# Kernel tuning notes

Measured on AMD Instinct MI355X. Metric: run time of the kernel, lower is better.

The kernel has to match this reference:

```python
import jax, jax.numpy as jnp
import numpy as np

N_NODES = 100000
EPS = 1e-12  # torch F.normalize eps


def setup_inputs() -> dict:
    key = jax.random.key(0)
    ks = jax.random.split(key, 8)
    F_IN, H, C, E = 128, 128, 8, 1600000
    s = 1.0 / np.sqrt(F_IN)
    return {
        "x": jax.random.normal(ks[0], (N_NODES, F_IN), dtype=jnp.float32),
        "edge_index": jax.random.randint(ks[1], (2, E), 0, N_NODES, dtype=jnp.int64),
        "W1": jax.random.normal(ks[2], (F_IN, H), dtype=jnp.float32) * s,
        "b1": jnp.zeros((H,), jnp.float32),
        "W2": jax.random.normal(ks[3], (H, H), dtype=jnp.float32) * s,
        "b2": jnp.zeros((H,), jnp.float32),
        "W3": jax.random.normal(ks[4], (H, H), dtype=jnp.float32) * s,
        "b3": jnp.zeros((H,), jnp.float32),
        "Wlin": jax.random.normal(ks[5], (3 * H, C), dtype=jnp.float32) * (1.0 / np.sqrt(3 * H)),
        "blin": jnp.zeros((C,), jnp.float32),
    }


def _gcn_norm(edge_index, n):
    # add self-loops, compute symmetric D^-1/2 A D^-1/2 edge weights
    loops = jnp.arange(n, dtype=edge_index.dtype)
    src = jnp.concatenate([edge_index[0], loops])
    dst = jnp.concatenate([edge_index[1], loops])
    deg = jax.ops.segment_sum(jnp.ones_like(dst, dtype=jnp.float32), dst, num_segments=n)
    dinv = jnp.where(deg > 0, jax.lax.rsqrt(deg), 0.0)
    norm = dinv[src] * dinv[dst]  # [E + N]
    return src, dst, norm


def _gcn_layer(x, W, b, src, dst, norm, n):
    h = x @ W                              # dense transform [N, H]
    msg = h[src] * norm[:, None]           # gather + scale  [E+N, H]
    agg = jax.ops.segment_sum(msg, dst, num_segments=n)  # scatter-add [N, H]
    h = jax.nn.relu(agg + b)
    nrm = jnp.sqrt(jnp.sum(h * h, axis=1, keepdims=True))
    return h / jnp.maximum(nrm, EPS)       # L2-normalize per node


def reference(x, edge_index, W1, b1, W2, b2, W3, b3, Wlin, blin):
    n = x.shape[0]
    src, dst, norm = _gcn_norm(edge_index, n)
    out1 = _gcn_layer(x, W1, b1, src, dst, norm, n)
    out2 = _gcn_layer(out1, W2, b2, src, dst, norm, n)
    out3 = _gcn_layer(out2, W3, b3, src, dst, norm, n)
    emb = jnp.concatenate([out1, out2, out3], axis=1)  # [N, 3H]
    logits = emb @ Wlin + blin
    return jax.nn.log_softmax(logits, axis=1)
```

## Files before the change

### kernel.cpp

```cpp
#include <hip/hip_runtime.h>
#include <math.h>


typedef __attribute__((ext_vector_type(8))) short short8;
typedef __attribute__((ext_vector_type(4))) float float4v;

__device__ __forceinline__ int edge_val(const int* e32, int is64, long long idx) {
  return is64 ? e32[idx * 2] : e32[idx];
}

__device__ __forceinline__ unsigned short f2bf(float f) {
  unsigned int u = __float_as_uint(f);
  u += 0x7fff + ((u >> 16) & 1);
  return (unsigned short)(u >> 16);
}

__device__ __forceinline__ float bf2f(unsigned short h) {
  return __uint_as_float((unsigned int)h << 16);
}

__device__ __forceinline__ float2 bfpair(unsigned int u) {
  return make_float2(__uint_as_float(u << 16), __uint_as_float(u & 0xffff0000u));
}

__global__ void prep_k(const int* e32, int* flag, int* counts, int* cursor, int n) {
  int stride = gridDim.x * blockDim.x;
  for (int j = blockIdx.x * blockDim.x + threadIdx.x; j < n; j += stride) {
    counts[j] = 0; cursor[j] = 0;
  }
  if (blockIdx.x == 0) {
    __shared__ int any;
    if (threadIdx.x == 0) any = 0;
    __syncthreads();
    int v = 0;
    for (int k = threadIdx.x; k < 4096; k += blockDim.x) v |= e32[2 * k + 1];
    if (v) atomicOr(&any, 1);
    __syncthreads();
    if (threadIdx.x == 0) *flag = (any == 0) ? 1 : 0;
  }
}

__global__ void count_k(const int* e32, const int* flag, int* counts, int E) {
  int is64 = *flag;
  long long i = (long long)blockIdx.x * blockDim.x + threadIdx.x;
  long long stride = (long long)gridDim.x * blockDim.x;
  for (; i < E; i += stride) {
    int d = edge_val(e32, is64, (long long)E + i);
    atomicAdd(&counts[d], 1);
  }
}

__global__ __launch_bounds__(1024) void scan1_k(const int* counts, int* partials,
                                                float* dinv, int n) {
  __shared__ int sb[1024];
  int i = blockIdx.x * 1024 + threadIdx.x;
  int v = (i < n) ? counts[i] : 0;
  if (i < n) dinv[i] = 1.0f / sqrtf((float)v + 1.0f);
  sb[threadIdx.x] = v;
  __syncthreads();
  for (int off = 512; off > 0; off >>= 1) {
    if (threadIdx.x < off) sb[threadIdx.x] += sb[threadIdx.x + off];
    __syncthreads();
  }
  if (threadIdx.x == 0) partials[blockIdx.x] = sb[0];
}

__global__ void scan2_k(int* partials, int nb) {
  if (blockIdx.x == 0 && threadIdx.x == 0) {
    int run = 0;
    for (int i = 0; i < nb; i++) { int v = partials[i]; partials[i] = run; run += v; }
  }
}

__global__ __launch_bounds__(1024) void scan3_k(const int* counts, const int* partials,
                                                int* row_ptr, int n) {
  __shared__ int sb[1024];
  int i = blockIdx.x * 1024 + threadIdx.x;
  int v = (i < n) ? counts[i] : 0;
  sb[threadIdx.x] = v;
  __syncthreads();
  for (int off = 1; off < 1024; off <<= 1) {
    int add = (threadIdx.x >= (unsigned)off) ? sb[threadIdx.x - off] : 0;
    __syncthreads();
    sb[threadIdx.x] += add;
    __syncthreads();
  }
  if (i < n) row_ptr[i] = partials[blockIdx.x] + sb[threadIdx.x] - v;
}

__global__ void fill_k(const int* e32, const int* flag, const int* row_ptr, int* cursor,
                       const float* dinv, int2* edata, int E) {
  int is64 = *flag;
  long long i = (long long)blockIdx.x * blockDim.x + threadIdx.x;
  long long stride = (long long)gridDim.x * blockDim.x;
  for (; i < E; i += stride) {
    int s = edge_val(e32, is64, i);
    int d = edge_val(e32, is64, (long long)E + i);
    int pos = atomicAdd(&cursor[d], 1);
    int idx = row_ptr[d] + pos;
    edata[idx] = make_int2(s, __float_as_int(dinv[s] * dinv[d]));
  }
}

__global__ void wconv_k(const float* __restrict__ W, unsigned short* __restrict__ Wt) {
  int t = blockIdx.x * blockDim.x + threadIdx.x;
  if (t >= 128 * 128) return;
  int col = t >> 7, k = t & 127;
  Wt[t] = f2bf(W[k * 128 + col]);
}

__global__ void xconv_k(const float* __restrict__ x, unsigned short* __restrict__ xb,
                        int total4) {
  int i = blockIdx.x * blockDim.x + threadIdx.x;
  int stride = gridDim.x * blockDim.x;
  for (; i < total4; i += stride) {
    float4 v = ((const float4*)x)[i];
    unsigned int u0 = (unsigned int)f2bf(v.x) | ((unsigned int)f2bf(v.y) << 16);
    unsigned int u1 = (unsigned int)f2bf(v.z) | ((unsigned int)f2bf(v.w) << 16);
    ((uint2*)xb)[i] = make_uint2(u0, u1);
  }
}

__global__ __launch_bounds__(256) void dense_mfma_k(
    const unsigned short* __restrict__ Xb, const unsigned short* __restrict__ Wt,
    unsigned short* __restrict__ Hout, int n) {
  int wave = threadIdx.x >> 6;
  int lane = threadIdx.x & 63;
  int row0 = blockIdx.x * 64 + wave * 16;
  int lm = lane & 15;
  int lk = lane >> 4;
  int arow = row0 + lm; if (arow >= n) arow = n - 1;
  const unsigned short* xp = Xb + (size_t)arow * 128 + lk * 8;
  short8 a[4];
#pragma unroll
  for (int kk = 0; kk < 4; kk++)
    a[kk] = *reinterpret_cast<const short8*>(xp + kk * 32);
#pragma unroll
  for (int nt = 0; nt < 8; nt++) {
    float4v acc = {0.f, 0.f, 0.f, 0.f};
    const unsigned short* wp = Wt + (size_t)(nt * 16 + lm) * 128 + lk * 8;
#pragma unroll
    for (int kk = 0; kk < 4; kk++) {
      short8 b = *reinterpret_cast<const short8*>(wp + kk * 32);
      acc = __builtin_amdgcn_mfma_f32_16x16x32_bf16(a[kk], b, acc, 0, 0, 0);
    }
    int col = nt * 16 + lm;
#pragma unroll
    for (int r = 0; r < 4; r++) {
      int row = row0 + lk * 4 + r;
      if (row < n) Hout[(size_t)row * 128 + col] = f2bf(acc[r]);
    }
  }
}

__global__ __launch_bounds__(256) void agg_k(const unsigned short* __restrict__ H,
                                             const int2* __restrict__ edata,
                                             const int* __restrict__ row_ptr,
                                             const int* __restrict__ counts,
                                             const float* __restrict__ dinv,
                                             const float* __restrict__ bias,
                                             unsigned short* __restrict__ Out, int n) {
  int node = blockIdx.x * 4 + (threadIdx.x >> 6);
  if (node >= n) return;
  int lane = threadIdx.x & 63;
  float di = dinv[node];
  float wself = di * di;
  unsigned int us = *(const unsigned int*)(H + (size_t)node * 128 + lane * 2);
  float2 hs = bfpair(us);
  float ax = hs.x * wself, ay = hs.y * wself;
  int start = row_ptr[node];
  int cnt = counts[node];
  for (int base = 0; base < cnt; base += 64) {
    int m = min(64, cnt - base);
    int2 me = (lane < m) ? edata[start + base + lane] : make_int2(0, 0);
    int i = 0;
    for (; i + 4 <= m; i += 4) {
      int s0 = __shfl(me.x, i),     s1 = __shfl(me.x, i + 1);
      int s2 = __shfl(me.x, i + 2), s3 = __shfl(me.x, i + 3);
      float w0 = __int_as_float(__shfl(me.y, i));
      float w1 = __int_as_float(__shfl(me.y, i + 1));
      float w2 = __int_as_float(__shfl(me.y, i + 2));
      float w3 = __int_as_float(__shfl(me.y, i + 3));
      unsigned int u0 = *(const unsigned int*)(H + (size_t)s0 * 128 + lane * 2);
      unsigned int u1 = *(const unsigned int*)(H + (size_t)s1 * 128 + lane * 2);
      unsigned int u2 = *(const unsigned int*)(H + (size_t)s2 * 128 + lane * 2);
      unsigned int u3 = *(const unsigned int*)(H + (size_t)s3 * 128 + lane * 2);
      float2 f0 = bfpair(u0), f1 = bfpair(u1), f2 = bfpair(u2), f3 = bfpair(u3);
      ax += f0.x * w0 + f1.x * w1 + f2.x * w2 + f3.x * w3;
      ay += f0.y * w0 + f1.y * w1 + f2.y * w2 + f3.y * w3;
    }
    for (; i < m; i++) {
      int s0 = __shfl(me.x, i);
      float w0 = __int_as_float(__shfl(me.y, i));
      float2 f0 = bfpair(*(const unsigned int*)(H + (size_t)s0 * 128 + lane * 2));
      ax += f0.x * w0;
      ay += f0.y * w0;
    }
  }
  float2 bv = *(const float2*)&bias[lane * 2];
  ax = fmaxf(ax + bv.x, 0.f);
  ay = fmaxf(ay + bv.y, 0.f);
  float ss = ax * ax + ay * ay;
#pragma unroll
  for (int off = 32; off > 0; off >>= 1) ss += __shfl_xor(ss, off);
  float scale = 1.0f / fmaxf(sqrtf(ss), 1e-12f);
  unsigned int po = (unsigned int)f2bf(ax * scale) | ((unsigned int)f2bf(ay * scale) << 16);
  *(unsigned int*)(Out + (size_t)node * 128 + lane * 2) = po;
}

__global__ __launch_bounds__(256) void final_k(const unsigned short* __restrict__ O1,
                                               const unsigned short* __restrict__ O2,
                                               const unsigned short* __restrict__ O3,
                                               const float* __restrict__ Wlin,
                                               const float* __restrict__ blin,
                                               float* __restrict__ out, int n) {
  __shared__ float Wl[384 * 8];
  __shared__ float bl[8];
  for (int i = threadIdx.x; i < 384 * 8 / 4; i += 256)
    ((float4*)Wl)[i] = ((const float4*)Wlin)[i];
  if (threadIdx.x < 8) bl[threadIdx.x] = blin[threadIdx.x];
  __syncthreads();
  int node = blockIdx.x * 256 + threadIdx.x;
  if (node >= n) return;
  float acc[8];
#pragma unroll
  for (int c = 0; c < 8; c++) acc[c] = bl[c];
  const unsigned short* parts[3] = {O1, O2, O3};
  for (int p = 0; p < 3; p++) {
    const uint2* e2 = (const uint2*)(parts[p] + (size_t)node * 128);
    for (int k4 = 0; k4 < 32; k4++) {
      uint2 v = e2[k4];
      float2 fa = bfpair(v.x), fb = bfpair(v.y);
      float vv[4] = {fa.x, fa.y, fb.x, fb.y};
      const float4* wr = (const float4*)&Wl[(p * 128 + k4 * 4) * 8];
#pragma unroll
      for (int j = 0; j < 4; j++) {
        float4 wa = wr[j * 2], wb = wr[j * 2 + 1];
        acc[0] += vv[j] * wa.x; acc[1] += vv[j] * wa.y;
        acc[2] += vv[j] * wa.z; acc[3] += vv[j] * wa.w;
        acc[4] += vv[j] * wb.x; acc[5] += vv[j] * wb.y;
        acc[6] += vv[j] * wb.z; acc[7] += vv[j] * wb.w;
      }
    }
  }
  float mx = acc[0];
#pragma unroll
  for (int c = 1; c < 8; c++) mx = fmaxf(mx, acc[c]);
  float se = 0.f;
#pragma unroll
  for (int c = 0; c < 8; c++) se += expf(acc[c] - mx);
  float lse = mx + logf(se);
  float* o = out + (size_t)node * 8;
#pragma unroll
  for (int c = 0; c < 8; c++) o[c] = acc[c] - lse;
}

extern "C" void kernel_launch(void* const* d_in, const int* in_sizes, int n_in,
                              void* d_out, int out_size, void* d_ws, size_t ws_size,
                              hipStream_t stream) {
  const float* x    = (const float*)d_in[0];
  const int*   e32  = (const int*)d_in[1];
  const float* W1   = (const float*)d_in[2];
  const float* b1   = (const float*)d_in[3];
  const float* W2   = (const float*)d_in[4];
  const float* b2   = (const float*)d_in[5];
  const float* W3   = (const float*)d_in[6];
  const float* b3   = (const float*)d_in[7];
  const float* Wlin = (const float*)d_in[8];
  const float* blin = (const float*)d_in[9];
  float* out = (float*)d_out;

  const int Nn = in_sizes[0] / 128;
  const int E  = in_sizes[1] / 2;

  char* ws = (char*)d_ws;
  size_t off = 0;
  auto take = [&](size_t bytes) -> char* {
    char* p = ws + off;
    off = (off + bytes + 255) & ~(size_t)255;
    return p;
  };
  int*   flag   = (int*)  take(256);
  int*   counts = (int*)  take((size_t)Nn * 4);
  int*   cursor = (int*)  take((size_t)Nn * 4);
  int*   rowp   = (int*)  take((size_t)Nn * 4);
  float* dinv   = (float*)take((size_t)Nn * 4);
  int*   parts  = (int*)  take(4096);
  int2*  edata  = (int2*) take((size_t)E * 8);
  unsigned short* xb  = (unsigned short*)take((size_t)Nn * 128 * 2);
  unsigned short* Hb  = (unsigned short*)take((size_t)Nn * 128 * 2);
  unsigned short* O1  = (unsigned short*)take((size_t)Nn * 128 * 2);
  unsigned short* O2  = (unsigned short*)take((size_t)Nn * 128 * 2);
  unsigned short* O3  = (unsigned short*)take((size_t)Nn * 128 * 2);
  unsigned short* Wt1 = (unsigned short*)take(128 * 128 * 2);
  unsigned short* Wt2 = (unsigned short*)take(128 * 128 * 2);
  unsigned short* Wt3 = (unsigned short*)take(128 * 128 * 2);

  int nb = (Nn + 1023) / 1024;
  int dense_grid = (Nn + 63) / 64;
  int agg_grid = (Nn + 3) / 4;

  hipLaunchKernelGGL(prep_k,  dim3(256),  dim3(256),  0, stream, e32, flag, counts, cursor, Nn);
  hipLaunchKernelGGL(count_k, dim3(2048), dim3(256),  0, stream, e32, flag, counts, E);
  hipLaunchKernelGGL(scan1_k, dim3(nb),   dim3(1024), 0, stream, counts, parts, dinv, Nn);
  hipLaunchKernelGGL(scan2_k, dim3(1),    dim3(1),    0, stream, parts, nb);
  hipLaunchKernelGGL(scan3_k, dim3(nb),   dim3(1024), 0, stream, counts, parts, rowp, Nn);
  hipLaunchKernelGGL(fill_k,  dim3(2048), dim3(256),  0, stream, e32, flag, rowp, cursor, dinv, edata, E);

  hipLaunchKernelGGL(wconv_k, dim3(64), dim3(256), 0, stream, W1, Wt1);
  hipLaunchKernelGGL(wconv_k, dim3(64), dim3(256), 0, stream, W2, Wt2);
  hipLaunchKernelGGL(wconv_k, dim3(64), dim3(256), 0, stream, W3, Wt3);
  hipLaunchKernelGGL(xconv_k, dim3(2048), dim3(256), 0, stream, x, xb, Nn * 32);

  hipLaunchKernelGGL(dense_mfma_k, dim3(dense_grid), dim3(256), 0, stream, xb, Wt1, Hb, Nn);
  hipLaunchKernelGGL(agg_k,        dim3(agg_grid),   dim3(256), 0, stream, Hb, edata, rowp, counts, dinv, b1, O1, Nn);
  hipLaunchKernelGGL(dense_mfma_k, dim3(dense_grid), dim3(256), 0, stream, O1, Wt2, Hb, Nn);
  hipLaunchKernelGGL(agg_k,        dim3(agg_grid),   dim3(256), 0, stream, Hb, edata, rowp, counts, dinv, b2, O2, Nn);
  hipLaunchKernelGGL(dense_mfma_k, dim3(dense_grid), dim3(256), 0, stream, O2, Wt3, Hb, Nn);
  hipLaunchKernelGGL(agg_k,        dim3(agg_grid),   dim3(256), 0, stream, Hb, edata, rowp, counts, dinv, b3, O3, Nn);
  hipLaunchKernelGGL(final_k, dim3((Nn + 255) / 256), dim3(256), 0, stream, O1, O2, O3, Wlin, blin, out, Nn);
}
```

Baseline: 605.8 us.

## Store dense-transform output in FP8 and recompute edge weights from dinv

The intermediate H produced by the dense MFMA transform is now stored as FP8 e4m3 instead of bf16, which halves the bytes gathered per edge in the aggregation kernel. The CSR edge array keeps only source indices, and each edge weight is recomputed in the aggregation as dinv[src]*dinv[dst], which halves edge-list traffic at the cost of an extra dinv gather. The three weight-conversion launches are merged into one. FP8 quantization of H adds notable numerical error, which risks exceeding the accuracy tolerance.

```diff
diff --git a/kernel.cpp b/kernel.cpp
--- a/kernel.cpp
+++ b/kernel.cpp
@@ -1,4 +1,5 @@
 #include <hip/hip_runtime.h>
+#include <hip/hip_fp8.h>
 #include <math.h>
 
 
@@ -15,12 +16,13 @@
   return (unsigned short)(u >> 16);
 }
 
-__device__ __forceinline__ float bf2f(unsigned short h) {
-  return __uint_as_float((unsigned int)h << 16);
-}
-
 __device__ __forceinline__ float2 bfpair(unsigned int u) {
   return make_float2(__uint_as_float(u << 16), __uint_as_float(u & 0xffff0000u));
+}
+
+__device__ __forceinline__ float2 fp8pair(unsigned short us) {
+  __hip_fp8x2_e4m3 p; p.__x = us;
+  return static_cast<float2>(p);
 }
 
 __global__ void prep_k(const int* e32, int* flag, int* counts, int* cursor, int n) {
@@ -89,7 +91,7 @@
 }
 
 __global__ void fill_k(const int* e32, const int* flag, const int* row_ptr, int* cursor,
-                       const float* dinv, int2* edata, int E) {
+                       int* esrc, int E) {
   int is64 = *flag;
   long long i = (long long)blockIdx.x * blockDim.x + threadIdx.x;
   long long stride = (long long)gridDim.x * blockDim.x;
@@ -97,15 +99,18 @@
     int s = edge_val(e32, is64, i);
     int d = edge_val(e32, is64, (long long)E + i);
     int pos = atomicAdd(&cursor[d], 1);
-    int idx = row_ptr[d] + pos;
-    edata[idx] = make_int2(s, __float_as_int(dinv[s] * dinv[d]));
-  }
-}
-
-__global__ void wconv_k(const float* __restrict__ W, unsigned short* __restrict__ Wt) {
+    esrc[row_ptr[d] + pos] = s;
+  }
+}
+
+__global__ void wconv_k(const float* __restrict__ W1, const float* __restrict__ W2,
+                        const float* __restrict__ W3, unsigned short* __restrict__ Wt) {
   int t = blockIdx.x * blockDim.x + threadIdx.x;
-  if (t >= 128 * 128) return;
-  int col = t >> 7, k = t & 127;
+  if (t >= 3 * 128 * 128) return;
+  int layer = t >> 14;
+  int r = t & 16383;
+  int col = r >> 7, k = r & 127;
+  const float* W = (layer == 0) ? W1 : (layer == 1) ? W2 : W3;
   Wt[t] = f2bf(W[k * 128 + col]);
 }
 
@@ -123,7 +128,7 @@
 
 __global__ __launch_bounds__(256) void dense_mfma_k(
     const unsigned short* __restrict__ Xb, const unsigned short* __restrict__ Wt,
-    unsigned short* __restrict__ Hout, int n) {
+    unsigned char* __restrict__ Hout, int n) {
   int wave = threadIdx.x >> 6;
   int lane = threadIdx.x & 63;
   int row0 = blockIdx.x * 64 + wave * 16;
@@ -148,13 +153,16 @@
 #pragma unroll
     for (int r = 0; r < 4; r++) {
       int row = row0 + lk * 4 + r;
-      if (row < n) Hout[(size_t)row * 128 + col] = f2bf(acc[r]);
-    }
-  }
-}
-
-__global__ __launch_bounds__(256) void agg_k(const unsigned short* __restrict__ H,
-                                             const int2* __restrict__ edata,
+      if (row < n) {
+        __hip_fp8_e4m3 q(acc[r]);
+        Hout[(size_t)row * 128 + col] = q.__x;
+      }
+    }
+  }
+}
+
+__global__ __launch_bounds__(256) void agg_k(const unsigned char* __restrict__ H,
+                                             const int* __restrict__ esrc,
                                              const int* __restrict__ row_ptr,
                                              const int* __restrict__ counts,
                                              const float* __restrict__ dinv,
@@ -164,35 +172,32 @@
   if (node >= n) return;
   int lane = threadIdx.x & 63;
   float di = dinv[node];
-  float wself = di * di;
-  unsigned int us = *(const unsigned int*)(H + (size_t)node * 128 + lane * 2);
-  float2 hs = bfpair(us);
-  float ax = hs.x * wself, ay = hs.y * wself;
+  float2 hs = fp8pair(*(const unsigned short*)(H + (size_t)node * 128 + lane * 2));
+  float ax = hs.x * di * di, ay = hs.y * di * di;
   int start = row_ptr[node];
   int cnt = counts[node];
   for (int base = 0; base < cnt; base += 64) {
     int m = min(64, cnt - base);
-    int2 me = (lane < m) ? edata[start + base + lane] : make_int2(0, 0);
+    int ms = (lane < m) ? esrc[start + base + lane] : 0;
+    float mw = dinv[ms] * di;
     int i = 0;
     for (; i + 4 <= m; i += 4) {
-      int s0 = __shfl(me.x, i),     s1 = __shfl(me.x, i + 1);
-      int s2 = __shfl(me.x, i + 2), s3 = __shfl(me.x, i + 3);
-      float w0 = __int_as_float(__shfl(me.y, i));
-      float w1 = __int_as_float(__shfl(me.y, i + 1));
-      float w2 = __int_as_float(__shfl(me.y, i + 2));
-      float w3 = __int_as_float(__shfl(me.y, i + 3));
-      unsigned int u0 = *(const unsigned int*)(H + (size_t)s0 * 128 + lane * 2);
-      unsigned int u1 = *(const unsigned int*)(H + (size_t)s1 * 128 + lane * 2);
-      unsigned int u2 = *(const unsigned int*)(H + (size_t)s2 * 128 + lane * 2);
-      unsigned int u3 = *(const unsigned int*)(H + (size_t)s3 * 128 + lane * 2);
-      float2 f0 = bfpair(u0), f1 = bfpair(u1), f2 = bfpair(u2), f3 = bfpair(u3);
+      int s0 = __shfl(ms, i),     s1 = __shfl(ms, i + 1);
+      int s2 = __shfl(ms, i + 2), s3 = __shfl(ms, i + 3);
+      float w0 = __shfl(mw, i),     w1 = __shfl(mw, i + 1);
+      float w2 = __shfl(mw, i + 2), w3 = __shfl(mw, i + 3);
+      unsigned short u0 = *(const unsigned short*)(H + (size_t)s0 * 128 + lane * 2);
+      unsigned short u1 = *(const unsigned short*)(H + (size_t)s1 * 128 + lane * 2);
+      unsigned short u2 = *(const unsigned short*)(H + (size_t)s2 * 128 + lane * 2);
+      unsigned short u3 = *(const unsigned short*)(H + (size_t)s3 * 128 + lane * 2);
+      float2 f0 = fp8pair(u0), f1 = fp8pair(u1), f2 = fp8pair(u2), f3 = fp8pair(u3);
       ax += f0.x * w0 + f1.x * w1 + f2.x * w2 + f3.x * w3;
       ay += f0.y * w0 + f1.y * w1 + f2.y * w2 + f3.y * w3;
     }
     for (; i < m; i++) {
-      int s0 = __shfl(me.x, i);
-      float w0 = __int_as_float(__shfl(me.y, i));
-      float2 f0 = bfpair(*(const unsigned int*)(H + (size_t)s0 * 128 + lane * 2));
+      int s0 = __shfl(ms, i);
+      float w0 = __shfl(mw, i);
+      float2 f0 = fp8pair(*(const unsigned short*)(H + (size_t)s0 * 128 + lane * 2));
       ax += f0.x * w0;
       ay += f0.y * w0;
     }
@@ -286,15 +291,13 @@
   int*   rowp   = (int*)  take((size_t)Nn * 4);
   float* dinv   = (float*)take((size_t)Nn * 4);
   int*   parts  = (int*)  take(4096);
-  int2*  edata  = (int2*) take((size_t)E * 8);
+  int*   esrc   = (int*)  take((size_t)E * 4);
   unsigned short* xb  = (unsigned short*)take((size_t)Nn * 128 * 2);
-  unsigned short* Hb  = (unsigned short*)take((size_t)Nn * 128 * 2);
+  unsigned char*  Hb  = (unsigned char*) take((size_t)Nn * 128);
   unsigned short* O1  = (unsigned short*)take((size_t)Nn * 128 * 2);
   unsigned short* O2  = (unsigned short*)take((size_t)Nn * 128 * 2);
   unsigned short* O3  = (unsigned short*)take((size_t)Nn * 128 * 2);
-  unsigned short* Wt1 = (unsigned short*)take(128 * 128 * 2);
-  unsigned short* Wt2 = (unsigned short*)take(128 * 128 * 2);
-  unsigned short* Wt3 = (unsigned short*)take(128 * 128 * 2);
+  unsigned short* Wt  = (unsigned short*)take(3 * 128 * 128 * 2);
 
   int nb = (Nn + 1023) / 1024;
   int dense_grid = (Nn + 63) / 64;
@@ -305,18 +308,16 @@
   hipLaunchKernelGGL(scan1_k, dim3(nb),   dim3(1024), 0, stream, counts, parts, dinv, Nn);
   hipLaunchKernelGGL(scan2_k, dim3(1),    dim3(1),    0, stream, parts, nb);
   hipLaunchKernelGGL(scan3_k, dim3(nb),   dim3(1024), 0, stream, counts, parts, rowp, Nn);
-  hipLaunchKernelGGL(fill_k,  dim3(2048), dim3(256),  0, stream, e32, flag, rowp, cursor, dinv, edata, E);
-
-  hipLaunchKernelGGL(wconv_k, dim3(64), dim3(256), 0, stream, W1, Wt1);
-  hipLaunchKernelGGL(wconv_k, dim3(64), dim3(256), 0, stream, W2, Wt2);
-  hipLaunchKernelGGL(wconv_k, dim3(64), dim3(256), 0, stream, W3, Wt3);
+  hipLaunchKernelGGL(fill_k,  dim3(2048), dim3(256),  0, stream, e32, flag, rowp, cursor, esrc, E);
+
+  hipLaunchKernelGGL(wconv_k, dim3(192),  dim3(256), 0, stream, W1, W2, W3, Wt);
   hipLaunchKernelGGL(xconv_k, dim3(2048), dim3(256), 0, stream, x, xb, Nn * 32);
 
-  hipLaunchKernelGGL(dense_mfma_k, dim3(dense_grid), dim3(256), 0, stream, xb, Wt1, Hb, Nn);
-  hipLaunchKernelGGL(agg_k,        dim3(agg_grid),   dim3(256), 0, stream, Hb, edata, rowp, counts, dinv, b1, O1, Nn);
-  hipLaunchKernelGGL(dense_mfma_k, dim3(dense_grid), dim3(256), 0, stream, O1, Wt2, Hb, Nn);
-  hipLaunchKernelGGL(agg_k,        dim3(agg_grid),   dim3(256), 0, stream, Hb, edata, rowp, counts, dinv, b2, O2, Nn);
-  hipLaunchKernelGGL(dense_mfma_k, dim3(dense_grid), dim3(256), 0, stream, O2, Wt3, Hb, Nn);
-  hipLaunchKernelGGL(agg_k,        dim3(agg_grid),   dim3(256), 0, stream, Hb, edata, rowp, counts, dinv, b3, O3, Nn);
+  hipLaunchKernelGGL(dense_mfma_k, dim3(dense_grid), dim3(256), 0, stream, xb, Wt,             Hb, Nn);
+  hipLaunchKernelGGL(agg_k,        dim3(agg_grid),   dim3(256), 0, stream, Hb, esrc, rowp, counts, dinv, b1, O1, Nn);
+  hipLaunchKernelGGL(dense_mfma_k, dim3(dense_grid), dim3(256), 0, stream, O1, Wt + 16384,     Hb, Nn);
+  hipLaunchKernelGGL(agg_k,        dim3(agg_grid),   dim3(256), 0, stream, Hb, esrc, rowp, counts, dinv, b2, O2, Nn);
+  hipLaunchKernelGGL(dense_mfma_k, dim3(dense_grid), dim3(256), 0, stream, O2, Wt + 32768,     Hb, Nn);
+  hipLaunchKernelGGL(agg_k,        dim3(agg_grid),   dim3(256), 0, stream, Hb, esrc, rowp, counts, dinv, b3, O3, Nn);
   hipLaunchKernelGGL(final_k, dim3((Nn + 255) / 256), dim3(256), 0, stream, O1, O2, O3, Wlin, blin, out, Nn);
 }
```

Result: no change. 616.5 us (+1.8%).
